# Optimization experiments

Measured on AMD Instinct MI355X. Metric: run time of the kernel, lower is better.

## Reference

```python
import math
import jax, jax.numpy as jnp
import numpy as np

MAX_N = 3; MAX_L = 3
CUTOFF = 5.0; TB_CUTOFF = 4.0; NBLOCKS = 3
N_NODES = 5000; N_EDGES = 60000; N_TRIP = 400000
NELEM = 89; DN = 128; DE = 128; UNITS = 128; DEG = MAX_N * MAX_L

# zeros of spherical bessel j_l, l = 0..2, first 3 roots each
J_ROOTS = np.array([
    [3.141592653589793, 6.283185307179586, 9.42477796076938],
    [4.493409457909064, 7.725251836937707, 10.904121659428899],
    [5.763459196894550, 9.095011330476355, 12.322940970566582],
])

def _jl(l, x, xp):
    s, c = xp.sin(x), xp.cos(x)
    if l == 0:
        return s / x
    if l == 1:
        return s / x**2 - c / x
    if l == 2:
        return (3.0 / x**3 - 1.0 / x) * s - 3.0 * c / x**2
    return (15.0 / x**4 - 6.0 / x**2) * s - (15.0 / x**3 - 1.0 / x) * c

SBF_FACTOR = math.sqrt(2.0 / CUTOFF**3)
SBF_NORM = np.stack([np.abs(_jl(l + 1, J_ROOTS[l], np)) for l in range(MAX_L)])  # [3,3]

def sbf_expand(r):  # [n] -> [n, MAX_L*MAX_N], l-major (matches torch cat over l)
    cols = []
    for l in range(MAX_L):
        x = r[:, None] * (J_ROOTS[l] / CUTOFF)[None, :]
        cols.append(_jl(l, x, jnp) * (SBF_FACTOR / SBF_NORM[l])[None, :])
    return jnp.concatenate(cols, axis=1)

Y00 = 0.28209479177387814  # 0.5*sqrt(1/pi)
Y10 = 0.4886025119029199   # sqrt(3/(4pi))
Y20 = 0.31539156525252005  # 0.25*sqrt(5/pi)

def shf_expand(cos_t):  # [n] -> [n, MAX_L]  real Y_l0(theta)
    return jnp.stack([jnp.full_like(cos_t, Y00), Y10 * cos_t, Y20 * (3.0 * cos_t**2 - 1.0)], axis=1)

def poly_cutoff(r, c):
    x = r / c
    return 1.0 - 6.0 * x**5 + 15.0 * x**4 - 10.0 * x**3

def gated_mlp(x, Ws, bs, gWs, gbs):
    h = x
    for W, b in zip(Ws, bs):
        h = jax.nn.silu(h @ W + b)
    g = x
    n = len(gWs)
    for i, (W, b) in enumerate(zip(gWs, gbs)):
        g = g @ W + b
        g = jax.nn.sigmoid(g) if i == n - 1 else jax.nn.silu(g)
    return h * g

def _forward(pos, node_type, src, dst, t_src, t_dst, emb_table, edge_emb_W, edge_emb_b,
             tb_atom_W, tb_atom_b, tb_bond_W, tb_bond_Wg,
             W0, b0, W1, b1, W2, b2, gW0, gb0, gW1, gb1, gW2, gb2, wt,
             fW0, fb0, fW1, fb1, fW2, fb2):
    n_nodes = pos.shape[0]; n_edges = src.shape[0]
    bond_vec = pos[dst] - pos[src]                              # [E,3]
    bond_dist = jnp.sqrt(jnp.sum(bond_vec**2, axis=1) + 1e-12)  # [E]
    rbf = sbf_expand(bond_dist)                                 # [E,9]
    # triplet (line-graph edge) geometry
    v1, v2 = bond_vec[t_src], bond_vec[t_dst]
    cos_t = jnp.sum(v1 * v2, axis=1) / (bond_dist[t_src] * bond_dist[t_dst])
    three_basis = sbf_expand(bond_dist[t_dst]) * jnp.repeat(shf_expand(cos_t), MAX_N, axis=1)  # [T,9]
    cut3 = poly_cutoff(bond_dist, TB_CUTOFF)
    tw = (cut3[t_src] * cut3[t_dst])[:, None]                   # [T,1]
    end_atom = dst[t_dst]                                       # [T]
    node_feat = emb_table[node_type]                            # [N,DN]
    edge_feat = jax.nn.silu(rbf @ edge_emb_W + edge_emb_b)      # [E,DE]
    for k in range(NBLOCKS):
        # --- three-body interaction ---
        atoms = jax.nn.sigmoid(node_feat @ tb_atom_W[k] + tb_atom_b[k])  # [N,9]
        basis = three_basis * atoms[end_atom] * tw                        # [T,9]
        nb = jax.ops.segment_sum(basis, t_src, num_segments=n_edges)      # [E,9]
        edge_feat = edge_feat + jax.nn.silu(nb @ tb_bond_W[k]) * jax.nn.sigmoid(nb @ tb_bond_Wg[k])
        # --- graph conv: edge update ---
        x = jnp.concatenate([node_feat[src], node_feat[dst], edge_feat], axis=1)  # [E,384]
        e_upd = gated_mlp(x, (W0[k, 0], W1[k, 0], W2[k, 0]), (b0[k, 0], b1[k, 0], b2[k, 0]),
                          (gW0[k, 0], gW1[k, 0], gW2[k, 0]), (gb0[k, 0], gb1[k, 0], gb2[k, 0])) * (rbf @ wt[k, 0])
        edge_feat = edge_feat + e_upd
        # --- graph conv: node update (sum messages at destination) ---
        x = jnp.concatenate([node_feat[src], node_feat[dst], edge_feat], axis=1)
        mess = gated_mlp(x, (W0[k, 1], W1[k, 1], W2[k, 1]), (b0[k, 1], b1[k, 1], b2[k, 1]),
                         (gW0[k, 1], gW1[k, 1], gW2[k, 1]), (gb0[k, 1], gb1[k, 1], gb2[k, 1])) * (rbf @ wt[k, 1])
        node_feat = node_feat + jax.ops.segment_sum(mess, dst, num_segments=n_nodes)
    # ReduceReadOut('mean') over nodes (single graph) + final MLP
    v = jnp.mean(node_feat, axis=0)
    h = jax.nn.silu(v @ fW0 + fb0)
    h = jax.nn.silu(h @ fW1 + fb1)
    return jnp.squeeze(h @ fW2 + fb2)

def setup_inputs() -> dict:
    key = jax.random.key(0)
    ks = iter(jax.random.split(key, 64))
    def nrm(shape, fan_in):
        return jax.random.normal(next(ks), shape, dtype=jnp.float32) / math.sqrt(float(fan_in))
    pos = jax.random.normal(next(ks), (N_NODES, 3), dtype=jnp.float32) * 1.5
    node_type = jax.random.randint(next(ks), (N_NODES,), 0, NELEM, dtype=jnp.int32)
    src = jax.random.randint(next(ks), (N_EDGES,), 0, N_NODES, dtype=jnp.int32)
    dst = (src + 1 + jax.random.randint(next(ks), (N_EDGES,), 0, N_NODES - 1, dtype=jnp.int32)) % N_NODES
    t_src = jax.random.randint(next(ks), (N_TRIP,), 0, N_EDGES, dtype=jnp.int32)
    t_dst = jax.random.randint(next(ks), (N_TRIP,), 0, N_EDGES, dtype=jnp.int32)
    DIN = 2 * DN + DE
    z = lambda *s: jnp.zeros(s, jnp.float32)
    return dict(
        pos=pos, node_type=node_type, src=src, dst=dst, t_src=t_src, t_dst=t_dst,
        emb_table=nrm((NELEM, DN), 1.0),
        edge_emb_W=nrm((DEG, DE), DEG), edge_emb_b=z(DE),
        tb_atom_W=nrm((NBLOCKS, DN, DEG), DN), tb_atom_b=z(NBLOCKS, DEG),
        tb_bond_W=nrm((NBLOCKS, DEG, DE), DEG), tb_bond_Wg=nrm((NBLOCKS, DEG, DE), DEG),
        W0=nrm((NBLOCKS, 2, DIN, UNITS), DIN), b0=z(NBLOCKS, 2, UNITS),
        W1=nrm((NBLOCKS, 2, UNITS, UNITS), UNITS), b1=z(NBLOCKS, 2, UNITS),
        W2=nrm((NBLOCKS, 2, UNITS, DE), UNITS), b2=z(NBLOCKS, 2, DE),
        gW0=nrm((NBLOCKS, 2, DIN, UNITS), DIN), gb0=z(NBLOCKS, 2, UNITS),
        gW1=nrm((NBLOCKS, 2, UNITS, UNITS), UNITS), gb1=z(NBLOCKS, 2, UNITS),
        gW2=nrm((NBLOCKS, 2, UNITS, DE), UNITS), gb2=z(NBLOCKS, 2, DE),
        wt=nrm((NBLOCKS, 2, DEG, DE), DEG),
        fW0=nrm((DN, UNITS), DN), fb0=z(UNITS),
        fW1=nrm((UNITS, UNITS), UNITS), fb1=z(UNITS),
        fW2=nrm((UNITS, 1), UNITS), fb2=z(1))

def reference(pos, node_type, src, dst, t_src, t_dst, emb_table, edge_emb_W, edge_emb_b,
              tb_atom_W, tb_atom_b, tb_bond_W, tb_bond_Wg,
              W0, b0, W1, b1, W2, b2, gW0, gb0, gW1, gb1, gW2, gb2, wt,
              fW0, fb0, fW1, fb1, fW2, fb2):
    return _forward(pos, node_type, src, dst, t_src, t_dst, emb_table, edge_emb_W, edge_emb_b,
                    tb_atom_W, tb_atom_b, tb_bond_W, tb_bond_Wg,
                    W0, b0, W1, b1, W2, b2, gW0, gb0, gW1, gb1, gW2, gb2, wt,
                    fW0, fb0, fW1, fb1, fW2, fb2)
```

## Files before the change

kernel.cpp:

```cpp
#include <hip/hip_runtime.h>
#include <stdint.h>

typedef __attribute__((ext_vector_type(8))) short bf16x8;
typedef __attribute__((ext_vector_type(4))) float f32x4;
typedef __attribute__((ext_vector_type(4))) uint32_t u32x4;
typedef unsigned short ushort;

#define XSS 392
#define HSS 144
#define TE 32

__device__ __forceinline__ float sigm(float x) { return __fdividef(1.0f, 1.0f + __expf(-x)); }
__device__ __forceinline__ float silu(float x) { return __fdividef(x, 1.0f + __expf(-x)); }
__device__ __forceinline__ short f2bf(float f) {
  uint32_t u = __float_as_uint(f);
  u = (u + 0x7fffu + ((u >> 16) & 1u)) >> 16;
  return (short)u;
}
__device__ __forceinline__ uint32_t cvt2(float lo, float hi) {
  uint32_t d;
  asm("v_cvt_pk_bf16_f32 %0, %1, %2" : "=v"(d) : "v"(lo), "v"(hi));
  return d;
}
__device__ __forceinline__ short f2bf1(float f) { return (short)cvt2(f, f); }

__device__ __forceinline__ float jl_eval(int l, float x) {
  float s, c;
  sincosf(x, &s, &c);
  float ix = 1.0f / x, ix2 = ix * ix;
  if (l == 0) return s * ix;
  if (l == 1) return s * ix2 - c * ix;
  if (l == 2) return (3.0f * ix2 * ix - ix) * s - 3.0f * ix2 * c;
  return (15.0f * ix2 * ix2 - 6.0f * ix2) * s - (15.0f * ix2 * ix - ix) * c;
}

__global__ void setup1_kernel(const int* __restrict__ ntb, const float* __restrict__ emb,
                              float* __restrict__ nf, int N,
                              const float* __restrict__ pos, const int* __restrict__ src,
                              const int* __restrict__ dst, float* __restrict__ bvec,
                              float* __restrict__ bdist, float* __restrict__ rbf,
                              float* __restrict__ cut3, int E,
                              const int* __restrict__ t_src, int* __restrict__ cnt_e,
                              int* __restrict__ cnt_n, int T) {
  int i = blockIdx.x * 256 + threadIdx.x;
  if (i < N * 128) {
    int n = i >> 7, c = i & 127;
    nf[i] = emb[ntb[n] * 128 + c];
  }
  if (i < E) {
    int s = src[i], d = dst[i];
    float dx = pos[d * 3 + 0] - pos[s * 3 + 0];
    float dy = pos[d * 3 + 1] - pos[s * 3 + 1];
    float dz = pos[d * 3 + 2] - pos[s * 3 + 2];
    float r = sqrtf(dx * dx + dy * dy + dz * dz + 1e-12f);
    bvec[i * 3 + 0] = dx; bvec[i * 3 + 1] = dy; bvec[i * 3 + 2] = dz;
    bdist[i] = r;
    const float roots[3][3] = {
        {3.141592653589793f, 6.283185307179586f, 9.42477796076938f},
        {4.493409457909064f, 7.725251836937707f, 10.904121659428899f},
        {5.763459196894550f, 9.095011330476355f, 12.322940970566582f}};
#pragma unroll
    for (int l = 0; l < 3; ++l) {
#pragma unroll
      for (int n = 0; n < 3; ++n) {
        float root = roots[l][n];
        float x = r * (root * 0.2f);
        float norm;
        if (l == 0) norm = 1.0f / root;
        else if (l == 1) norm = 1.0f / sqrtf(1.0f + root * root);
        else {
          float t = 3.0f * root / (3.0f - root * root);
          norm = fabsf(t - root) / (root * root * sqrtf(1.0f + t * t));
        }
        rbf[i * 9 + l * 3 + n] = jl_eval(l, x) * (0.12649110640673518f / norm);
      }
    }
    float xx = r * 0.25f;
    float x3 = xx * xx * xx;
    cut3[i] = 1.0f - 6.0f * x3 * xx * xx + 15.0f * x3 * xx - 10.0f * x3;
    atomicAdd(&cnt_n[d], 1);
  }
  if (i < T) atomicAdd(&cnt_e[t_src[i]], 1);
}

__device__ void scan_chunk(const int* __restrict__ in, int* __restrict__ incl,
                           int* __restrict__ bsum, int L, int b) {
  __shared__ int sm[256];
  int i = b * 256 + threadIdx.x;
  int v = i < L ? in[i] : 0;
  sm[threadIdx.x] = v;
  __syncthreads();
  for (int st = 1; st < 256; st <<= 1) {
    int t = threadIdx.x >= st ? sm[threadIdx.x - st] : 0;
    __syncthreads();
    sm[threadIdx.x] += t;
    __syncthreads();
  }
  if (i < L) incl[i] = sm[threadIdx.x];
  if (threadIdx.x == 255) bsum[b] = sm[255];
}

__global__ void setup2_kernel(const float* __restrict__ rbf, const float* __restrict__ eW,
                              const float* __restrict__ eB, float* __restrict__ ef, int E,
                              const int* __restrict__ cnt_e, int* __restrict__ incl_e,
                              int* __restrict__ bsum_e, int ebk,
                              const int* __restrict__ cnt_n, int* __restrict__ incl_n,
                              int* __restrict__ bsum_n, int nbk, int N,
                              const float* __restrict__ nf, const float* __restrict__ taW,
                              const float* __restrict__ taB, float* __restrict__ atoms) {
  int b = blockIdx.x;
  if (b < ebk) scan_chunk(cnt_e, incl_e, bsum_e, E, b);
  else if (b < ebk + nbk) scan_chunk(cnt_n, incl_n, bsum_n, N, b - ebk);
  int i = b * 256 + threadIdx.x;
  if (i < E * 128) {
    int e = i >> 7, c = i & 127;
    float acc = eB[c];
#pragma unroll
    for (int d = 0; d < 9; ++d) acc += rbf[e * 9 + d] * eW[d * 128 + c];
    ef[i] = silu(acc);
  }
  if (i < N * 9) {
    int n = i / 9, d = i - n * 9;
    float acc = taB[d];
    for (int c = 0; c < 128; ++c) acc += nf[n * 128 + c] * taW[c * 9 + d];
    atoms[i] = sigm(acc);
  }
}

__global__ void scan_top2_kernel(int* __restrict__ bsum_e, int ne, int* __restrict__ bsum_n,
                                 int nn) {
  __shared__ int sm[1024];
  int* bs = blockIdx.x == 0 ? bsum_e : bsum_n;
  int nb = blockIdx.x == 0 ? ne : nn;
  int tid = threadIdx.x;
  int orig = tid < nb ? bs[tid] : 0;
  sm[tid] = orig;
  __syncthreads();
  for (int st = 1; st < 1024; st <<= 1) {
    int t = tid >= st ? sm[tid - st] : 0;
    __syncthreads();
    sm[tid] += t;
    __syncthreads();
  }
  if (tid < nb) bs[tid] = sm[tid] - orig;
}

__global__ void fin2_kernel(const int* __restrict__ cnt_e, const int* __restrict__ incl_e,
                            const int* __restrict__ bsum_e, int ebk, int* __restrict__ off_e,
                            int* __restrict__ cur_e, int E, const int* __restrict__ cnt_n,
                            const int* __restrict__ incl_n, const int* __restrict__ bsum_n,
                            int* __restrict__ off_n, int* __restrict__ cur_n, int N) {
  int b = blockIdx.x;
  if (b < ebk) {
    int i = b * 256 + threadIdx.x;
    if (i < E) {
      int o = incl_e[i] - cnt_e[i] + bsum_e[b];
      off_e[i] = o; cur_e[i] = o;
    }
  } else {
    int bb = b - ebk;
    int i = bb * 256 + threadIdx.x;
    if (i < N) {
      int o = incl_n[i] - cnt_n[i] + bsum_n[bb];
      off_n[i] = o; cur_n[i] = o;
    }
  }
}

__global__ void build_kernel(const int* __restrict__ t_src, const int* __restrict__ t_dst,
                             const int* __restrict__ dst, const float* __restrict__ bvec,
                             const float* __restrict__ bdist, const float* __restrict__ rbf,
                             const float* __restrict__ cut3, int* __restrict__ cur_e,
                             float* __restrict__ stbp, int* __restrict__ sa, int T,
                             int* __restrict__ cur_n, int* __restrict__ invp, int E) {
  int t = blockIdx.x * 256 + threadIdx.x;
  if (t < T) {
    int i = t_src[t], j = t_dst[t];
    float ax = bvec[i * 3], ay = bvec[i * 3 + 1], az = bvec[i * 3 + 2];
    float bx = bvec[j * 3], by = bvec[j * 3 + 1], bz = bvec[j * 3 + 2];
    float ct = (ax * bx + ay * by + az * bz) / (bdist[i] * bdist[j]);
    float tw = cut3[i] * cut3[j];
    float sh[3];
    sh[0] = 0.28209479177387814f * tw;
    sh[1] = 0.4886025119029199f * ct * tw;
    sh[2] = 0.31539156525252005f * (3.0f * ct * ct - 1.0f) * tw;
    int pos = atomicAdd(&cur_e[i], 1);
#pragma unroll
    for (int l = 0; l < 3; ++l)
#pragma unroll
      for (int n = 0; n < 3; ++n)
        stbp[(size_t)pos * 9 + l * 3 + n] = rbf[j * 9 + l * 3 + n] * sh[l];
    sa[pos] = dst[j];
  }
  if (t < E) {
    int pos = atomicAdd(&cur_n[dst[t]], 1);
    invp[t] = pos;
  }
}

__device__ void pack_one(const float* __restrict__ Wf, short* __restrict__ Wp, int K, int rr) {
  int per = 8 * (K / 32) * 64;
  int u = rr / per, r2 = rr - u * per;
  int lane = r2 & 63, tile = r2 >> 6;
  int kt = tile % (K / 32), nt = tile / (K / 32);
  int n = nt * 16 + (lane & 15);
  int k0 = kt * 32 + (lane >> 4) * 8;
  const float* s = Wf + (size_t)u * K * 128;
  bf16x8 v;
#pragma unroll
  for (int e = 0; e < 8; ++e) v[e] = f2bf(s[(size_t)(k0 + e) * 128 + n]);
  *(bf16x8*)(Wp + (size_t)u * K * 128 + (size_t)tile * 512 + lane * 8) = v;
}

__device__ void pack_pad9(const float* __restrict__ s, short* __restrict__ dp9, int l2) {
  int lane = l2 & 63, tile = l2 >> 6;
  int n = tile * 16 + (lane & 15);
  int k0 = (lane >> 4) * 8;
  bf16x8 v;
#pragma unroll
  for (int e = 0; e < 8; ++e)
    v[e] = (k0 + e < 9) ? f2bf(s[(size_t)(k0 + e) * 128 + n]) : (short)0;
  *(bf16x8*)(dp9 + tile * 512 + lane * 8) = v;
}

__global__ void pack_all_kernel(const float* __restrict__ W0, const float* __restrict__ G0,
                                const float* __restrict__ W1, const float* __restrict__ G1,
                                const float* __restrict__ W2, const float* __restrict__ G2,
                                const float* __restrict__ tbW, const float* __restrict__ tbG,
                                const float* __restrict__ WT,
                                short* __restrict__ pW0, short* __restrict__ pG0,
                                short* __restrict__ pW1, short* __restrict__ pG1,
                                short* __restrict__ pW2, short* __restrict__ pG2,
                                short* __restrict__ ptbW, short* __restrict__ ptbG,
                                short* __restrict__ pWT) {
  int idx = blockIdx.x * 256 + threadIdx.x;
  const int t384 = 6 * 8 * 12 * 64, t128 = 6 * 8 * 4 * 64;
  if (idx < t384) { pack_one(W0, pW0, 384, idx); return; }
  if (idx < 2 * t384) { pack_one(G0, pG0, 384, idx - t384); return; }
  int j = idx - 2 * t384;
  if (j < t128) { pack_one(W1, pW1, 128, j); return; }
  if (j < 2 * t128) { pack_one(G1, pG1, 128, j - t128); return; }
  if (j < 3 * t128) { pack_one(W2, pW2, 128, j - 2 * t128); return; }
  if (j < 4 * t128) { pack_one(G2, pG2, 128, j - 3 * t128); return; }
  j -= 4 * t128;
  if (j < 3072) {
    int kb = j >> 10;
    int w2 = (j >> 9) & 1;
    int l2 = j & 511;
    const float* s = (w2 ? tbG : tbW) + (size_t)kb * 9 * 128;
    short* dp = (w2 ? ptbG : ptbW) + (size_t)kb * 4096;
    pack_pad9(s, dp, l2);
    return;
  }
  j -= 3072;
  if (j < 3072) {
    int u = j >> 9;
    pack_pad9(WT + (size_t)u * 9 * 128, pWT + (size_t)u * 4096, j & 511);
  }
}

__device__ __forceinline__ f32x4 mfma16(bf16x8 a, bf16x8 b, f32x4 c) {
  return __builtin_amdgcn_mfma_f32_16x16x32_bf16(a, b, c, 0, 0, 0);
}

__device__ __forceinline__ void store_hg(short* hsb, short* gsb, int wave, int lane,
                                         const f32x4 (&aW)[2], const f32x4 (&aG)[2]) {
  const int lrow = lane & 15, lk = lane >> 4;
  const int colx = (wave * 16 + lrow) ^ (lk * 40);
#pragma unroll
  for (int mt = 0; mt < 2; ++mt)
#pragma unroll
    for (int rg = 0; rg < 4; ++rg) {
      int row = mt * 16 + lk * 4 + rg;
      hsb[row * HSS + colx] = f2bf1(silu(aW[mt][rg]));
      gsb[row * HSS + colx] = f2bf1(silu(aG[mt][rg]));
    }
}

__device__ __forceinline__ void layer128w(const short* hin, const short* gin,
                                          const short* __restrict__ pW,
                                          const short* __restrict__ pG,
                                          const float* __restrict__ Bh,
                                          const float* __restrict__ Bg, int wave, int lane,
                                          f32x4 (&aW)[2], f32x4 (&aG)[2]) {
  const int lrow = lane & 15, lk = lane >> 4;
  const int s0 = (lrow >> 2) & 3;
  float bw = Bh[wave * 16 + lrow], bg = Bg[wave * 16 + lrow];
  aW[0] = {bw, bw, bw, bw}; aW[1] = aW[0];
  aG[0] = {bg, bg, bg, bg}; aG[1] = aG[0];
#pragma unroll
  for (int kt = 0; kt < 4; ++kt) {
    int aoff = (kt * 32 + lk * 8) ^ (s0 * 40);
    bf16x8 ah0 = *(const bf16x8*)(hin + (size_t)lrow * HSS + aoff);
    bf16x8 ah1 = *(const bf16x8*)(hin + (size_t)(16 + lrow) * HSS + aoff);
    bf16x8 ag0 = *(const bf16x8*)(gin + (size_t)lrow * HSS + aoff);
    bf16x8 ag1 = *(const bf16x8*)(gin + (size_t)(16 + lrow) * HSS + aoff);
    bf16x8 bw8 = *(const bf16x8*)(pW + (size_t)(wave * 4 + kt) * 512 + lane * 8);
    bf16x8 bg8 = *(const bf16x8*)(pG + (size_t)(wave * 4 + kt) * 512 + lane * 8);
    aW[0] = mfma16(ah0, bw8, aW[0]);
    aW[1] = mfma16(ah1, bw8, aW[1]);
    aG[0] = mfma16(ag0, bg8, aG[0]);
    aG[1] = mfma16(ag1, bg8, aG[1]);
  }
}

__device__ __forceinline__ void run_chain(
    const short* xsb, short* hsb, short* gsb,
    const short* __restrict__ pW0, const short* __restrict__ pG0,
    const short* __restrict__ pW1, const short* __restrict__ pG1,
    const short* __restrict__ pW2, const short* __restrict__ pG2,
    const float* __restrict__ B0, const float* __restrict__ Gb0,
    const float* __restrict__ B1, const float* __restrict__ Gb1,
    const float* __restrict__ B2, const float* __restrict__ Gb2,
    int wave, int lane, f32x4 (&aW)[2], f32x4 (&aG)[2]) {
  const int lrow = lane & 15, lk = lane >> 4;
  const int s0 = (lrow >> 2) & 3;
  {
    float bw = B0[wave * 16 + lrow], bg = Gb0[wave * 16 + lrow];
    aW[0] = {bw, bw, bw, bw}; aW[1] = aW[0];
    aG[0] = {bg, bg, bg, bg}; aG[1] = aG[0];
  }
#pragma unroll
  for (int kt = 0; kt < 12; ++kt) {
    int al = kt * 32 + lk * 8;
    int aoff = (al < 256) ? al : (256 + ((al - 256) ^ (s0 << 4)));
    bf16x8 a0 = *(const bf16x8*)(xsb + (size_t)lrow * XSS + aoff);
    bf16x8 a1 = *(const bf16x8*)(xsb + (size_t)(16 + lrow) * XSS + aoff);
    bf16x8 bw8 = *(const bf16x8*)(pW0 + (size_t)(wave * 12 + kt) * 512 + lane * 8);
    bf16x8 bg8 = *(const bf16x8*)(pG0 + (size_t)(wave * 12 + kt) * 512 + lane * 8);
    aW[0] = mfma16(a0, bw8, aW[0]);
    aW[1] = mfma16(a1, bw8, aW[1]);
    aG[0] = mfma16(a0, bg8, aG[0]);
    aG[1] = mfma16(a1, bg8, aG[1]);
  }
  store_hg(hsb, gsb, wave, lane, aW, aG);
  __syncthreads();
  layer128w(hsb, gsb, pW1, pG1, B1, Gb1, wave, lane, aW, aG);
  __syncthreads();
  store_hg(hsb, gsb, wave, lane, aW, aG);
  __syncthreads();
  layer128w(hsb, gsb, pW2, pG2, B2, Gb2, wave, lane, aW, aG);
}

__global__ __launch_bounds__(512, 6) void gmlp_fused(
    const float* __restrict__ nf, float* __restrict__ ef, const float* __restrict__ rbf,
    const int* __restrict__ src, const int* __restrict__ dst,
    const float* __restrict__ stbp, const int* __restrict__ sa,
    const int* __restrict__ off_e, const int* __restrict__ cnt_e,
    const float* __restrict__ atoms, const int* __restrict__ invp,
    const short* __restrict__ ptbW, const short* __restrict__ ptbG,
    const short* __restrict__ pW0a, const short* __restrict__ pG0a,
    const short* __restrict__ pW1a, const short* __restrict__ pG1a,
    const short* __restrict__ pW2a, const short* __restrict__ pG2a,
    const float* __restrict__ B0a, const float* __restrict__ Gb0a,
    const float* __restrict__ B1a, const float* __restrict__ Gb1a,
    const float* __restrict__ B2a, const float* __restrict__ Gb2a,
    const short* __restrict__ pWTa,
    const short* __restrict__ pW0b, const short* __restrict__ pG0b,
    const short* __restrict__ pW1b, const short* __restrict__ pG1b,
    const short* __restrict__ pW2b, const short* __restrict__ pG2b,
    const float* __restrict__ B0b, const float* __restrict__ Gb0b,
    const float* __restrict__ B1b, const float* __restrict__ Gb1b,
    const float* __restrict__ B2b, const float* __restrict__ Gb2b,
    const short* __restrict__ pWTb,
    float* __restrict__ mbuf, int E, int writeEf) {
  __shared__ __align__(16) short xs[32][XSS];
  __shared__ __align__(16) short hs[32 * HSS];
  __shared__ __align__(16) short gs[32 * HSS];
  __shared__ __align__(16) short nbl[32][40];
  __shared__ __align__(16) short rbl[32][40];
  __shared__ int invs[32];
  const int tid = threadIdx.x;
  const int e0 = blockIdx.x * TE;
  const int r = tid >> 4, q = tid & 15;
  int eg = e0 + r; if (eg >= E) eg = E - 1;

  {
    float acc = 0.f;
    if (q < 9) {
      int o = off_e[eg], c = cnt_e[eg];
      for (int pp = o; pp < o + c; ++pp)
        acc += stbp[(size_t)pp * 9 + q] * atoms[(size_t)sa[pp] * 9 + q];
    }
    nbl[r][q] = (q < 9) ? f2bf1(acc) : (short)0;
    nbl[r][q + 16] = 0;
  }
  {
    const float* sp0 = nf + (size_t)src[eg] * 128;
    const float* sp1 = nf + (size_t)dst[eg] * 128;
#pragma unroll
    for (int seg = 0; seg < 2; ++seg) {
      const float* sp = seg == 0 ? sp0 : sp1;
      float4 f0 = *(const float4*)(sp + q * 8);
      float4 f1 = *(const float4*)(sp + q * 8 + 4);
      u32x4 v = {cvt2(f0.x, f0.y), cvt2(f0.z, f0.w), cvt2(f1.x, f1.y), cvt2(f1.z, f1.w)};
      *(u32x4*)&xs[r][seg * 128 + q * 8] = v;
    }
    for (int idx = tid; idx < 32 * 32; idx += 512) {
      int rr = idx >> 5, d = idx & 31;
      int ee = e0 + rr; if (ee >= E) ee = E - 1;
      rbl[rr][d] = (d < 9) ? f2bf1(rbf[ee * 9 + d]) : (short)0;
    }
    if (tid < 32) {
      int ee = e0 + tid; if (ee >= E) ee = E - 1;
      invs[tid] = invp[ee];
    }
  }
  __syncthreads();

  const int wave = tid >> 6;
  const int lane = tid & 63;
  const int lrow = lane & 15, lk = lane >> 4;
  const int col = wave * 16 + lrow;
  const int cs = 256 + (col ^ (lk << 4));
  f32x4 aW[2], aG[2];
  float efb[2][4];

  {
    bf16x8 ta0 = *(const bf16x8*)&nbl[lrow][lk * 8];
    bf16x8 ta1 = *(const bf16x8*)&nbl[16 + lrow][lk * 8];
    bf16x8 tbw = *(const bf16x8*)(ptbW + wave * 512 + lane * 8);
    bf16x8 tbg = *(const bf16x8*)(ptbG + wave * 512 + lane * 8);
    f32x4 z = {0.f, 0.f, 0.f, 0.f};
    f32x4 tW0 = mfma16(ta0, tbw, z), tW1 = mfma16(ta1, tbw, z);
    f32x4 tG0 = mfma16(ta0, tbg, z), tG1 = mfma16(ta1, tbg, z);
#pragma unroll
    for (int mt = 0; mt < 2; ++mt)
#pragma unroll
      for (int rg = 0; rg < 4; ++rg) {
        int row = mt * 16 + lk * 4 + rg;
        int ec = e0 + row; if (ec >= E) ec = E - 1;
        float tw = mt == 0 ? tW0[rg] : tW1[rg];
        float tg = mt == 0 ? tG0[rg] : tG1[rg];
        float base = ef[(size_t)ec * 128 + col] + silu(tw) * sigm(tg);
        efb[mt][rg] = base;
        xs[row][cs] = f2bf1(base);
      }
  }
  __syncthreads();

  run_chain(&xs[0][0], hs, gs, pW0a, pG0a, pW1a, pG1a, pW2a, pG2a,
            B0a, Gb0a, B1a, Gb1a, B2a, Gb2a, wave, lane, aW, aG);
  {
    bf16x8 ra0 = *(const bf16x8*)&rbl[lrow][lk * 8];
    bf16x8 ra1 = *(const bf16x8*)&rbl[16 + lrow][lk * 8];
    bf16x8 wtb = *(const bf16x8*)(pWTa + wave * 512 + lane * 8);
    f32x4 z = {0.f, 0.f, 0.f, 0.f};
    f32x4 wv0 = mfma16(ra0, wtb, z), wv1 = mfma16(ra1, wtb, z);
#pragma unroll
    for (int mt = 0; mt < 2; ++mt)
#pragma unroll
      for (int rg = 0; rg < 4; ++rg) {
        int row = mt * 16 + lk * 4 + rg;
        int e = e0 + row;
        float wv = mt == 0 ? wv0[rg] : wv1[rg];
        float v = silu(aW[mt][rg]) * sigm(aG[mt][rg]) * wv;
        float nv = efb[mt][rg] + v;
        if (e < E && writeEf) ef[(size_t)e * 128 + col] = nv;
        xs[row][cs] = f2bf1(nv);
      }
  }
  __syncthreads();

  run_chain(&xs[0][0], hs, gs, pW0b, pG0b, pW1b, pG1b, pW2b, pG2b,
            B0b, Gb0b, B1b, Gb1b, B2b, Gb2b, wave, lane, aW, aG);
  {
    bf16x8 ra0 = *(const bf16x8*)&rbl[lrow][lk * 8];
    bf16x8 ra1 = *(const bf16x8*)&rbl[16 + lrow][lk * 8];
    bf16x8 wtb = *(const bf16x8*)(pWTb + wave * 512 + lane * 8);
    f32x4 z = {0.f, 0.f, 0.f, 0.f};
    f32x4 wv0 = mfma16(ra0, wtb, z), wv1 = mfma16(ra1, wtb, z);
#pragma unroll
    for (int mt = 0; mt < 2; ++mt)
#pragma unroll
      for (int rg = 0; rg < 4; ++rg) {
        int row = mt * 16 + lk * 4 + rg;
        int e = e0 + row;
        float wv = mt == 0 ? wv0[rg] : wv1[rg];
        float v = silu(aW[mt][rg]) * sigm(aG[mt][rg]) * wv;
        if (e < E) mbuf[(size_t)invs[row] * 128 + col] = v;
      }
  }
}

__global__ void node_gather_kernel(float* __restrict__ nf, const float* __restrict__ mbuf,
                                   const int* __restrict__ off_n, const int* __restrict__ cnt_n,
                                   const float* __restrict__ taW, const float* __restrict__ taB,
                                   float* __restrict__ atoms, int N, int doAtoms) {
  __shared__ float red[2][9][128];
  int half = threadIdx.x >> 7, c = threadIdx.x & 127;
  int n = blockIdx.x * 2 + half;
  float v = 0.f;
  if (n < N) {
    int o = off_n[n], cnt = cnt_n[n];
    float acc = 0.f;
    for (int p = 0; p < cnt; ++p) acc += mbuf[(size_t)(o + p) * 128 + c];
    v = nf[(size_t)n * 128 + c] + acc;
    nf[(size_t)n * 128 + c] = v;
  }
  if (doAtoms) {
#pragma unroll
    for (int d = 0; d < 9; ++d) red[half][d][c] = (n < N) ? v * taW[c * 9 + d] : 0.f;
    for (int s = 64; s >= 1; s >>= 1) {
      __syncthreads();
      for (int idx = threadIdx.x; idx < 2 * 9 * s; idx += 256) {
        int h = idx / (9 * s), rem = idx - h * 9 * s;
        int d = rem / s, j = rem - d * s;
        red[h][d][j] += red[h][d][j + s];
      }
    }
    __syncthreads();
    if (threadIdx.x < 18) {
      int h = threadIdx.x / 9, d = threadIdx.x - h * 9;
      int nn = blockIdx.x * 2 + h;
      if (nn < N) atoms[nn * 9 + d] = sigm(red[h][d][0] + taB[d]);
    }
  }
}

__global__ void mean_kernel(const float* __restrict__ nf, float* __restrict__ partial, int N) {
  __shared__ float sm[256];
  int n0 = blockIdx.x * 256;
  int col = threadIdx.x & 127, half = threadIdx.x >> 7;
  int nend = n0 + 256 < N ? n0 + 256 : N;
  float s = 0.f;
  for (int n = n0 + half; n < nend; n += 2) s += nf[n * 128 + col];
  sm[threadIdx.x] = s;
  __syncthreads();
  if (threadIdx.x < 128)
    partial[blockIdx.x * 128 + threadIdx.x] = sm[threadIdx.x] + sm[threadIdx.x + 128];
}

__global__ void final_kernel(const float* __restrict__ partial, int nchunks, float Nf,
                             const float* __restrict__ fW0, const float* __restrict__ fb0,
                             const float* __restrict__ fW1, const float* __restrict__ fb1,
                             const float* __restrict__ fW2, const float* __restrict__ fb2,
                             float* __restrict__ out) {
  __shared__ float v[128], h[128], red[128];
  int tid = threadIdx.x;
  float s = 0.f;
  for (int b = 0; b < nchunks; ++b) s += partial[b * 128 + tid];
  v[tid] = s / Nf;
  __syncthreads();
  float acc = fb0[tid];
  for (int c = 0; c < 128; ++c) acc += v[c] * fW0[c * 128 + tid];
  h[tid] = silu(acc);
  __syncthreads();
  acc = fb1[tid];
  for (int c = 0; c < 128; ++c) acc += h[c] * fW1[c * 128 + tid];
  __syncthreads();
  v[tid] = silu(acc);
  __syncthreads();
  red[tid] = v[tid] * fW2[tid];
  __syncthreads();
  for (int st = 64; st > 0; st >>= 1) {
    if (tid < st) red[tid] += red[tid + st];
    __syncthreads();
  }
  if (tid == 0) out[0] = red[0] + fb2[0];
}

extern "C" void kernel_launch(void* const* d_in, const int* in_sizes, int n_in,
                              void* d_out, int out_size, void* d_ws, size_t ws_size,
                              hipStream_t stream) {
  const float* pos = (const float*)d_in[0];
  const int* node_type = (const int*)d_in[1];
  const int* src = (const int*)d_in[2];
  const int* dst = (const int*)d_in[3];
  const int* t_src = (const int*)d_in[4];
  const int* t_dst = (const int*)d_in[5];
  const float* emb = (const float*)d_in[6];
  const float* eW = (const float*)d_in[7];
  const float* eB = (const float*)d_in[8];
  const float* taW = (const float*)d_in[9];
  const float* taB = (const float*)d_in[10];
  const float* tbW = (const float*)d_in[11];
  const float* tbG = (const float*)d_in[12];
  const float* W0 = (const float*)d_in[13]; const float* B0 = (const float*)d_in[14];
  const float* W1 = (const float*)d_in[15]; const float* B1 = (const float*)d_in[16];
  const float* W2 = (const float*)d_in[17]; const float* B2 = (const float*)d_in[18];
  const float* G0 = (const float*)d_in[19]; const float* Gb0 = (const float*)d_in[20];
  const float* G1 = (const float*)d_in[21]; const float* Gb1 = (const float*)d_in[22];
  const float* G2 = (const float*)d_in[23]; const float* Gb2 = (const float*)d_in[24];
  const float* WT = (const float*)d_in[25];
  const float* fW0 = (const float*)d_in[26]; const float* fb0 = (const float*)d_in[27];
  const float* fW1 = (const float*)d_in[28]; const float* fb1 = (const float*)d_in[29];
  const float* fW2 = (const float*)d_in[30]; const float* fb2 = (const float*)d_in[31];

  const int N = in_sizes[1];
  const int E = in_sizes[2];
  const int T = in_sizes[4];

  char* p = (char*)d_ws;
  auto alloc = [&](size_t bytes) -> char* {
    char* r = p;
    p += (bytes + 255) & ~(size_t)255;
    return r;
  };
  float*  nf    = (float*)alloc((size_t)N * 128 * 4);
  float*  ef    = (float*)alloc((size_t)E * 128 * 4);
  float*  mbuf  = (float*)alloc((size_t)E * 128 * 4);
  float*  rbf   = (float*)alloc((size_t)E * 9 * 4);
  float*  bvec  = (float*)alloc((size_t)E * 3 * 4);
  float*  bdist = (float*)alloc((size_t)E * 4);
  float*  cut3  = (float*)alloc((size_t)E * 4);
  float*  stbp  = (float*)alloc((size_t)T * 9 * 4);
  int*    sa    = (int*)alloc((size_t)T * 4);
  float*  atoms = (float*)alloc((size_t)N * 9 * 4);
  float*  part  = (float*)alloc((size_t)64 * 128 * 4);
  int* cnt_all = (int*)alloc((size_t)(E + N) * 4);
  int* cnt_e = cnt_all, *cnt_n = cnt_all + E;
  int* incl_e = (int*)alloc((size_t)E * 4);
  int* incl_n = (int*)alloc((size_t)N * 4);
  int* off_e  = (int*)alloc((size_t)E * 4);
  int* off_n  = (int*)alloc((size_t)N * 4);
  int* cur_e  = (int*)alloc((size_t)E * 4);
  int* cur_n  = (int*)alloc((size_t)N * 4);
  int* invp   = (int*)alloc((size_t)E * 4);
  int* bsum_e = (int*)alloc((size_t)1024 * 4);
  int* bsum_n = (int*)alloc((size_t)1024 * 4);
  short* pW0s = (short*)alloc((size_t)6 * 384 * 128 * 2);
  short* pG0s = (short*)alloc((size_t)6 * 384 * 128 * 2);
  short* pW1s = (short*)alloc((size_t)6 * 128 * 128 * 2);
  short* pG1s = (short*)alloc((size_t)6 * 128 * 128 * 2);
  short* pW2s = (short*)alloc((size_t)6 * 128 * 128 * 2);
  short* pG2s = (short*)alloc((size_t)6 * 128 * 128 * 2);
  short* ptbWs = (short*)alloc((size_t)3 * 4096 * 2);
  short* ptbGs = (short*)alloc((size_t)3 * 4096 * 2);
  short* pWTs  = (short*)alloc((size_t)6 * 4096 * 2);
  (void)ws_size; (void)n_in; (void)out_size;

  const int ebk = (E + 255) / 256, nbk = (N + 255) / 256;

  pack_all_kernel<<<504, 256, 0, stream>>>(W0, G0, W1, G1, W2, G2, tbW, tbG, WT,
                                           pW0s, pG0s, pW1s, pG1s, pW2s, pG2s,
                                           ptbWs, ptbGs, pWTs);
  hipMemsetAsync(cnt_all, 0, (size_t)(E + N) * 4, stream);
  {
    int g1 = N * 128; if (E > g1) g1 = E; if (T > g1) g1 = T;
    setup1_kernel<<<(g1 + 255) / 256, 256, 0, stream>>>(
        node_type, emb, nf, N, pos, src, dst, bvec, bdist, rbf, cut3, E, t_src, cnt_e, cnt_n, T);
  }
  {
    int g2 = E * 128; int g2b = (ebk + nbk) * 256; if (g2b > g2) g2 = g2b;
    if (N * 9 > g2) g2 = N * 9;
    setup2_kernel<<<(g2 + 255) / 256, 256, 0, stream>>>(
        rbf, eW, eB, ef, E, cnt_e, incl_e, bsum_e, ebk, cnt_n, incl_n, bsum_n, nbk, N,
        nf, taW, taB, atoms);
  }
  scan_top2_kernel<<<2, 1024, 0, stream>>>(bsum_e, ebk, bsum_n, nbk);
  fin2_kernel<<<ebk + nbk, 256, 0, stream>>>(cnt_e, incl_e, bsum_e, ebk, off_e, cur_e, E,
                                             cnt_n, incl_n, bsum_n, off_n, cur_n, N);
  {
    int g3 = T > E ? T : E;
    build_kernel<<<(g3 + 255) / 256, 256, 0, stream>>>(t_src, t_dst, dst, bvec, bdist, rbf,
                                                       cut3, cur_e, stbp, sa, T, cur_n, invp, E);
  }

  const int gblocks = (E + TE - 1) / TE;
  for (int k = 0; k < 3; ++k) {
    size_t u0 = (size_t)(k * 2 + 0), u1 = u0 + 1;
    gmlp_fused<<<gblocks, 512, 0, stream>>>(
        nf, ef, rbf, src, dst, stbp, sa, off_e, cnt_e, atoms, invp,
        ptbWs + (size_t)k * 4096, ptbGs + (size_t)k * 4096,
        pW0s + u0 * 384 * 128, pG0s + u0 * 384 * 128, pW1s + u0 * 128 * 128,
        pG1s + u0 * 128 * 128, pW2s + u0 * 128 * 128, pG2s + u0 * 128 * 128,
        B0 + u0 * 128, Gb0 + u0 * 128, B1 + u0 * 128, Gb1 + u0 * 128, B2 + u0 * 128,
        Gb2 + u0 * 128, pWTs + u0 * 4096,
        pW0s + u1 * 384 * 128, pG0s + u1 * 384 * 128, pW1s + u1 * 128 * 128,
        pG1s + u1 * 128 * 128, pW2s + u1 * 128 * 128, pG2s + u1 * 128 * 128,
        B0 + u1 * 128, Gb0 + u1 * 128, B1 + u1 * 128, Gb1 + u1 * 128, B2 + u1 * 128,
        Gb2 + u1 * 128, pWTs + u1 * 4096,
        mbuf, E, k < 2 ? 1 : 0);
    int nk = k < 2 ? k + 1 : 0;
    node_gather_kernel<<<(N + 1) / 2, 256, 0, stream>>>(
        nf, mbuf, off_n, cnt_n, taW + (size_t)nk * 128 * 9, taB + (size_t)nk * 9,
        atoms, N, k < 2 ? 1 : 0);
  }

  int nchunks = (N + 255) / 256;
  mean_kernel<<<nchunks, 256, 0, stream>>>(nf, part, N);
  final_kernel<<<1, 128, 0, stream>>>(part, nchunks, (float)N, fW0, fb0, fW1, fb1, fW2, fb2,
                                      (float*)d_out);
}
```

Before: 513.0 us.

## Fuse edge embedding into first gated-MLP block via MFMA

Removes the elementwise edge-embedding computation (rbf @ eW + bias, silu) from setup2_kernel and computes it inside the k=0 gmlp_fused launch with a bf16 MFMA, using a newly packed eW. This avoids writing and then re-reading the E x 128 fp32 edge feature buffer in the first block, and shrinks the setup2 grid from E*128 threads to just the scan and atom work. The cost is bf16 rounding of rbf and eW in the embedding, plus an extra branch and a few MFMAs in the fused kernel.

```diff
diff --git a/kernel.cpp b/kernel.cpp
--- a/kernel.cpp
+++ b/kernel.cpp
@@ -100,10 +100,8 @@
   if (threadIdx.x == 255) bsum[b] = sm[255];
 }
 
-__global__ void setup2_kernel(const float* __restrict__ rbf, const float* __restrict__ eW,
-                              const float* __restrict__ eB, float* __restrict__ ef, int E,
-                              const int* __restrict__ cnt_e, int* __restrict__ incl_e,
-                              int* __restrict__ bsum_e, int ebk,
+__global__ void setup2_kernel(const int* __restrict__ cnt_e, int* __restrict__ incl_e,
+                              int* __restrict__ bsum_e, int ebk, int E,
                               const int* __restrict__ cnt_n, int* __restrict__ incl_n,
                               int* __restrict__ bsum_n, int nbk, int N,
                               const float* __restrict__ nf, const float* __restrict__ taW,
@@ -112,13 +110,6 @@
   if (b < ebk) scan_chunk(cnt_e, incl_e, bsum_e, E, b);
   else if (b < ebk + nbk) scan_chunk(cnt_n, incl_n, bsum_n, N, b - ebk);
   int i = b * 256 + threadIdx.x;
-  if (i < E * 128) {
-    int e = i >> 7, c = i & 127;
-    float acc = eB[c];
-#pragma unroll
-    for (int d = 0; d < 9; ++d) acc += rbf[e * 9 + d] * eW[d * 128 + c];
-    ef[i] = silu(acc);
-  }
   if (i < N * 9) {
     int n = i / 9, d = i - n * 9;
     float acc = taB[d];
@@ -227,12 +218,12 @@
                                 const float* __restrict__ W1, const float* __restrict__ G1,
                                 const float* __restrict__ W2, const float* __restrict__ G2,
                                 const float* __restrict__ tbW, const float* __restrict__ tbG,
-                                const float* __restrict__ WT,
+                                const float* __restrict__ WT, const float* __restrict__ eW,
                                 short* __restrict__ pW0, short* __restrict__ pG0,
                                 short* __restrict__ pW1, short* __restrict__ pG1,
                                 short* __restrict__ pW2, short* __restrict__ pG2,
                                 short* __restrict__ ptbW, short* __restrict__ ptbG,
-                                short* __restrict__ pWT) {
+                                short* __restrict__ pWT, short* __restrict__ peW) {
   int idx = blockIdx.x * 256 + threadIdx.x;
   const int t384 = 6 * 8 * 12 * 64, t128 = 6 * 8 * 4 * 64;
   if (idx < t384) { pack_one(W0, pW0, 384, idx); return; }
@@ -256,7 +247,10 @@
   if (j < 3072) {
     int u = j >> 9;
     pack_pad9(WT + (size_t)u * 9 * 128, pWT + (size_t)u * 4096, j & 511);
-  }
+    return;
+  }
+  j -= 3072;
+  if (j < 512) pack_pad9(eW, peW, j);
 }
 
 __device__ __forceinline__ f32x4 mfma16(bf16x8 a, bf16x8 b, f32x4 c) {
@@ -349,6 +343,7 @@
     const int* __restrict__ off_e, const int* __restrict__ cnt_e,
     const float* __restrict__ atoms, const int* __restrict__ invp,
     const short* __restrict__ ptbW, const short* __restrict__ ptbG,
+    const short* __restrict__ peW, const float* __restrict__ eB,
     const short* __restrict__ pW0a, const short* __restrict__ pG0a,
     const short* __restrict__ pW1a, const short* __restrict__ pG1a,
     const short* __restrict__ pW2a, const short* __restrict__ pG2a,
@@ -363,7 +358,7 @@
     const float* __restrict__ B1b, const float* __restrict__ Gb1b,
     const float* __restrict__ B2b, const float* __restrict__ Gb2b,
     const short* __restrict__ pWTb,
-    float* __restrict__ mbuf, int E, int writeEf) {
+    float* __restrict__ mbuf, int E, int writeEf, int isK0) {
   __shared__ __align__(16) short xs[32][XSS];
   __shared__ __align__(16) short hs[32 * HSS];
   __shared__ __align__(16) short gs[32 * HSS];
@@ -424,15 +419,27 @@
     f32x4 z = {0.f, 0.f, 0.f, 0.f};
     f32x4 tW0 = mfma16(ta0, tbw, z), tW1 = mfma16(ta1, tbw, z);
     f32x4 tG0 = mfma16(ta0, tbg, z), tG1 = mfma16(ta1, tbg, z);
+    f32x4 e0v = z, e1v = z;
+    if (isK0) {
+      bf16x8 ra0 = *(const bf16x8*)&rbl[lrow][lk * 8];
+      bf16x8 ra1 = *(const bf16x8*)&rbl[16 + lrow][lk * 8];
+      bf16x8 ew8 = *(const bf16x8*)(peW + wave * 512 + lane * 8);
+      float ebv = eB[col];
+      f32x4 ec = {ebv, ebv, ebv, ebv};
+      e0v = mfma16(ra0, ew8, ec);
+      e1v = mfma16(ra1, ew8, ec);
+    }
 #pragma unroll
     for (int mt = 0; mt < 2; ++mt)
 #pragma unroll
       for (int rg = 0; rg < 4; ++rg) {
         int row = mt * 16 + lk * 4 + rg;
-        int ec = e0 + row; if (ec >= E) ec = E - 1;
+        int ec2 = e0 + row; if (ec2 >= E) ec2 = E - 1;
         float tw = mt == 0 ? tW0[rg] : tW1[rg];
         float tg = mt == 0 ? tG0[rg] : tG1[rg];
-        float base = ef[(size_t)ec * 128 + col] + silu(tw) * sigm(tg);
+        float base_ef = isK0 ? silu(mt == 0 ? e0v[rg] : e1v[rg])
+                             : ef[(size_t)ec2 * 128 + col];
+        float base = base_ef + silu(tw) * sigm(tg);
         efb[mt][rg] = base;
         xs[row][cs] = f2bf1(base);
       }
@@ -628,13 +635,14 @@
   short* ptbWs = (short*)alloc((size_t)3 * 4096 * 2);
   short* ptbGs = (short*)alloc((size_t)3 * 4096 * 2);
   short* pWTs  = (short*)alloc((size_t)6 * 4096 * 2);
+  short* peWs  = (short*)alloc((size_t)4096 * 2);
   (void)ws_size; (void)n_in; (void)out_size;
 
   const int ebk = (E + 255) / 256, nbk = (N + 255) / 256;
 
-  pack_all_kernel<<<504, 256, 0, stream>>>(W0, G0, W1, G1, W2, G2, tbW, tbG, WT,
+  pack_all_kernel<<<506, 256, 0, stream>>>(W0, G0, W1, G1, W2, G2, tbW, tbG, WT, eW,
                                            pW0s, pG0s, pW1s, pG1s, pW2s, pG2s,
-                                           ptbWs, ptbGs, pWTs);
+                                           ptbWs, ptbGs, pWTs, peWs);
   hipMemsetAsync(cnt_all, 0, (size_t)(E + N) * 4, stream);
   {
     int g1 = N * 128; if (E > g1) g1 = E; if (T > g1) g1 = T;
@@ -642,11 +650,9 @@
         node_type, emb, nf, N, pos, src, dst, bvec, bdist, rbf, cut3, E, t_src, cnt_e, cnt_n, T);
   }
   {
-    int g2 = E * 128; int g2b = (ebk + nbk) * 256; if (g2b > g2) g2 = g2b;
-    if (N * 9 > g2) g2 = N * 9;
+    int g2 = (ebk + nbk) * 256; if (N * 9 > g2) g2 = N * 9;
     setup2_kernel<<<(g2 + 255) / 256, 256, 0, stream>>>(
-        rbf, eW, eB, ef, E, cnt_e, incl_e, bsum_e, ebk, cnt_n, incl_n, bsum_n, nbk, N,
-        nf, taW, taB, atoms);
+        cnt_e, incl_e, bsum_e, ebk, E, cnt_n, incl_n, bsum_n, nbk, N, nf, taW, taB, atoms);
   }
   scan_top2_kernel<<<2, 1024, 0, stream>>>(bsum_e, ebk, bsum_n, nbk);
   fin2_kernel<<<ebk + nbk, 256, 0, stream>>>(cnt_e, incl_e, bsum_e, ebk, off_e, cur_e, E,
@@ -662,7 +668,7 @@
     size_t u0 = (size_t)(k * 2 + 0), u1 = u0 + 1;
     gmlp_fused<<<gblocks, 512, 0, stream>>>(
         nf, ef, rbf, src, dst, stbp, sa, off_e, cnt_e, atoms, invp,
-        ptbWs + (size_t)k * 4096, ptbGs + (size_t)k * 4096,
+        ptbWs + (size_t)k * 4096, ptbGs + (size_t)k * 4096, peWs, eB,
         pW0s + u0 * 384 * 128, pG0s + u0 * 384 * 128, pW1s + u0 * 128 * 128,
         pG1s + u0 * 128 * 128, pW2s + u0 * 128 * 128, pG2s + u0 * 128 * 128,
         B0 + u0 * 128, Gb0 + u0 * 128, B1 + u0 * 128, Gb1 + u0 * 128, B2 + u0 * 128,
@@ -671,7 +677,7 @@
         pG1s + u1 * 128 * 128, pW2s + u1 * 128 * 128, pG2s + u1 * 128 * 128,
         B0 + u1 * 128, Gb0 + u1 * 128, B1 + u1 * 128, Gb1 + u1 * 128, B2 + u1 * 128,
         Gb2 + u1 * 128, pWTs + u1 * 4096,
-        mbuf, E, k < 2 ? 1 : 0);
+        mbuf, E, k < 2 ? 1 : 0, k == 0 ? 1 : 0);
     int nk = k < 2 ? k + 1 : 0;
     node_gather_kernel<<<(N + 1) / 2, 256, 0, stream>>>(
         nf, mbuf, off_n, cnt_n, taW + (size_t)nk * 128 * 9, taB + (size_t)nk * 9,
```

Result: no change. 514.6 us (+0.3%).
